# Optimization experiments

Measured on AMD Instinct MI355X. Metric: run time of the kernel, lower is better.

The kernel has to match this reference:

```python
import jax, jax.numpy as jnp
import numpy as np

D_I = 1024
D_O = 1024
B = 4
S = 4096

def setup_inputs() -> dict:
    key = jax.random.key(0)
    kx, kq, kk, kv = jax.random.split(key, 4)
    x = jax.random.normal(kx, (B, S, D_I), dtype=jnp.float32)
    # torch Linear(d_i, d_o) weight is [d_o, d_i]; we store transposed [d_i, d_o]
    sc = 1.0 / np.sqrt(D_I)
    Wq = jax.random.uniform(kq, (D_I, D_O), jnp.float32, -sc, sc)
    Wk = jax.random.uniform(kk, (D_I, D_O), jnp.float32, -sc, sc)
    Wv = jax.random.uniform(kv, (D_I, D_O), jnp.float32, -sc, sc)
    return {"x": x, "Wq": Wq, "Wk": Wk, "Wv": Wv}

def reference(x, Wq, Wk, Wv):
    # x: [B, S, d_i]
    q = jnp.einsum('bsd,de->bse', x, Wq)  # [B,S,d_o]
    k = jnp.einsum('bsd,de->bse', x, Wk)
    v = jnp.einsum('bsd,de->bse', x, Wv)
    scores = jnp.einsum('bqe,bke->bqk', q, k)  # [B,S,S]
    S_len = x.shape[1]
    causal = jnp.tril(jnp.ones((S_len, S_len), dtype=bool))  # keep lower tri
    scores = jnp.where(causal[None], scores, -jnp.inf)
    attn = jax.nn.softmax(scores / jnp.sqrt(jnp.float32(v.shape[-1])), axis=-1)
    # dropout p=0.0 -> identity
    return jnp.einsum('bqk,bke->bqe', attn, v)  # [B,S,d_o]
```

## Files before the change

kernel.cpp:

```cpp
#include <hip/hip_runtime.h>

typedef __bf16 bf16x8 __attribute__((ext_vector_type(8)));
typedef float f32x4 __attribute__((ext_vector_type(4)));

#define B_SZ 4
#define S_SZ 4096
#define D_SZ 1024
#define ELEMS_MAT ((size_t)B_SZ * S_SZ * D_SZ)

#define OFF_Q  ((size_t)0)
#define OFF_K  (ELEMS_MAT)
#define OFF_VT (2 * ELEMS_MAT)
#define ZONE   (3 * ELEMS_MAT)
#define OFF_XB (ZONE)
#define OFF_V  (ZONE + ELEMS_MAT)
#define OFF_WT (ZONE + 2 * ELEMS_MAT)
#define OFF_S  (ZONE)
#define S_BATCH ((size_t)8912896)

#define MFMA16(a, b, c) __builtin_amdgcn_mfma_f32_16x16x32_bf16((a), (b), (c), 0, 0, 0)

static __device__ __forceinline__ unsigned short f2bf(float f) {
  __bf16 h = (__bf16)f;
  return __builtin_bit_cast(unsigned short, h);
}

static __device__ __forceinline__ void async_lds16(const void* g, void* l) {
  __builtin_amdgcn_global_load_lds((__attribute__((address_space(1))) void*)g,
                                   (__attribute__((address_space(3))) void*)l, 16, 0, 0);
}

__global__ void cast_x_kernel(const float* __restrict__ x, unsigned short* __restrict__ xb) {
  size_t i = ((size_t)blockIdx.x * 256 + threadIdx.x) * 8;
  f32x4 a = *(const f32x4*)(x + i);
  f32x4 b = *(const f32x4*)(x + i + 4);
  bf16x8 o;
  o[0] = (__bf16)a[0]; o[1] = (__bf16)a[1]; o[2] = (__bf16)a[2]; o[3] = (__bf16)a[3];
  o[4] = (__bf16)b[0]; o[5] = (__bf16)b[1]; o[6] = (__bf16)b[2]; o[7] = (__bf16)b[3];
  *(bf16x8*)(xb + i) = o;
}

__global__ void cast_wt_kernel(const float* __restrict__ Wq, const float* __restrict__ Wk,
                               const float* __restrict__ Wv, unsigned short* __restrict__ Wt) {
  __shared__ float tl[64][65];
  const float* W = blockIdx.z == 0 ? Wq : (blockIdx.z == 1 ? Wk : Wv);
  unsigned short* out = Wt + (size_t)blockIdx.z * (size_t)D_SZ * (size_t)D_SZ;
  const int k0 = blockIdx.x * 64, n0 = blockIdx.y * 64;
  const int t = threadIdx.x;
  for (int i = t; i < 4096; i += 256) {
    int r = i >> 6, c = i & 63;
    tl[r][c] = W[(size_t)(k0 + r) * D_SZ + n0 + c];
  }
  __syncthreads();
  for (int i = t; i < 4096; i += 256) {
    int r = i >> 6, c = i & 63;
    out[(size_t)(n0 + r) * D_SZ + k0 + c] = f2bf(tl[c][r]);
  }
}

static __device__ __forceinline__ bf16x8 lds_frag(const char* half, int r, int hi) {
  return *(const bf16x8*)(half + r * 64 + ((hi * 16) ^ (((r >> 1) & 3) << 4)));
}

static __device__ __forceinline__ void stage_half256(const char* src, size_t ld, char* lds, int tid) {
#pragma unroll
  for (int it = 0; it < 2; ++it) {
    int i = it * 512 + tid;
    int row = i >> 2;
    int s = (i & 3) ^ ((row >> 1) & 3);
    async_lds16(src + (size_t)row * ld + s * 16, lds + i * 16);
  }
}
static __device__ __forceinline__ void stage_half128(const char* src, size_t ld, char* lds, int tid) {
  int row = tid >> 2;
  int s = (tid & 3) ^ ((row >> 1) & 3);
  async_lds16(src + (size_t)row * ld + s * 16, lds + tid * 16);
}

static __device__ __forceinline__ void mainloop8p(const char* A, size_t lda,
                                                  const char* B, size_t ldb, int NT,
                                                  char sm[2][2][2][16384],
                                                  int tid, f32x4 acc[8][4]) {
  const int lane = tid & 63, w = tid >> 6;
  const int wm = w >> 2, wn = w & 3, lr = lane & 15, hi = lane >> 4;
  stage_half256(A,      lda, sm[0][0][0], tid);
  stage_half256(B,      ldb, sm[0][1][0], tid);
  stage_half256(A + 64, lda, sm[0][0][1], tid);
  stage_half256(B + 64, ldb, sm[0][1][1], tid);
  asm volatile("s_waitcnt vmcnt(4)" ::: "memory");
  __builtin_amdgcn_s_barrier();
  for (int t = 0; t < NT; ++t) {
    const int d = t & 1;
    const char* At1 = A + (size_t)(t + 1) * 128;
    const char* Bt1 = B + (size_t)(t + 1) * 128;
    const bool pre = (t + 1 < NT);
    bf16x8 af[4], bfr[4];
#pragma unroll
    for (int g = 0; g < 4; ++g) bfr[g] = lds_frag(sm[d][1][0], wn * 64 + g * 16 + lr, hi);
#pragma unroll
    for (int f = 0; f < 4; ++f) af[f] = lds_frag(sm[d][0][0], wm * 128 + f * 16 + lr, hi);
    if (pre) stage_half256(At1, lda, sm[d ^ 1][0][0], tid);
    __builtin_amdgcn_s_barrier();
    asm volatile("s_waitcnt lgkmcnt(0)" ::: "memory");
    __builtin_amdgcn_s_setprio(1);
#pragma unroll
    for (int f = 0; f < 4; ++f)
#pragma unroll
      for (int g = 0; g < 4; ++g) acc[f][g] = MFMA16(af[f], bfr[g], acc[f][g]);
    __builtin_amdgcn_s_setprio(0);
    __builtin_amdgcn_s_barrier();
#pragma unroll
    for (int f = 0; f < 4; ++f) af[f] = lds_frag(sm[d][0][0], wm * 128 + 64 + f * 16 + lr, hi);
    if (pre) stage_half256(Bt1, ldb, sm[d ^ 1][1][0], tid);
    __builtin_amdgcn_s_barrier();
    asm volatile("s_waitcnt lgkmcnt(0)" ::: "memory");
    __builtin_amdgcn_s_setprio(1);
#pragma unroll
    for (int f = 0; f < 4; ++f)
#pragma unroll
      for (int g = 0; g < 4; ++g) acc[4 + f][g] = MFMA16(af[f], bfr[g], acc[4 + f][g]);
    __builtin_amdgcn_s_setprio(0);
    if (pre) asm volatile("s_waitcnt vmcnt(4)" ::: "memory");
    else     asm volatile("s_waitcnt vmcnt(0)" ::: "memory");
    __builtin_amdgcn_s_barrier();
#pragma unroll
    for (int g = 0; g < 4; ++g) bfr[g] = lds_frag(sm[d][1][1], wn * 64 + g * 16 + lr, hi);
#pragma unroll
    for (int f = 0; f < 4; ++f) af[f] = lds_frag(sm[d][0][1], wm * 128 + f * 16 + lr, hi);
    if (pre) stage_half256(At1 + 64, lda, sm[d ^ 1][0][1], tid);
    __builtin_amdgcn_s_barrier();
    asm volatile("s_waitcnt lgkmcnt(0)" ::: "memory");
    __builtin_amdgcn_s_setprio(1);
#pragma unroll
    for (int f = 0; f < 4; ++f)
#pragma unroll
      for (int g = 0; g < 4; ++g) acc[f][g] = MFMA16(af[f], bfr[g], acc[f][g]);
    __builtin_amdgcn_s_setprio(0);
    __builtin_amdgcn_s_barrier();
#pragma unroll
    for (int f = 0; f < 4; ++f) af[f] = lds_frag(sm[d][0][1], wm * 128 + 64 + f * 16 + lr, hi);
    if (pre) stage_half256(Bt1 + 64, ldb, sm[d ^ 1][1][1], tid);
    __builtin_amdgcn_s_barrier();
    asm volatile("s_waitcnt lgkmcnt(0)" ::: "memory");
    __builtin_amdgcn_s_setprio(1);
#pragma unroll
    for (int f = 0; f < 4; ++f)
#pragma unroll
      for (int g = 0; g < 4; ++g) acc[4 + f][g] = MFMA16(af[f], bfr[g], acc[4 + f][g]);
    __builtin_amdgcn_s_setprio(0);
    if (pre) asm volatile("s_waitcnt vmcnt(4)" ::: "memory");
    __builtin_amdgcn_s_barrier();
  }
}

#define GEMM_PRE()                                    \
  __shared__ char sm[2][2][2][16384];                 \
  const int tid = threadIdx.x;                        \
  f32x4 acc[8][4];                                    \
  {                                                   \
    const f32x4 z4 = {0.f, 0.f, 0.f, 0.f};            \
    _Pragma("unroll") for (int f = 0; f < 8; ++f)     \
      _Pragma("unroll") for (int g = 0; g < 4; ++g)   \
        acc[f][g] = z4;                               \
  }

#define EPI_IDX()                                     \
  const int lane = tid & 63, w = tid >> 6;            \
  const int wm = w >> 2, wn = w & 3;                  \
  const int lr = lane & 15, hi = lane >> 4;

__global__ __launch_bounds__(512, 2) void gemm_qkv256(const unsigned short* __restrict__ xb,
                                                      const unsigned short* __restrict__ Wt,
                                                      unsigned short* __restrict__ Q,
                                                      unsigned short* __restrict__ K,
                                                      unsigned short* __restrict__ V) {
  GEMM_PRE();
  const int bid = blockIdx.x;
  const int sw = (bid & 7) * 96 + (bid >> 3);
  const int mt = sw % 64, nt = sw / 64;
  const char* A = (const char*)xb + (size_t)mt * 256 * 2048;
  const char* Bp = (const char*)Wt + (size_t)nt * 256 * 2048;
  mainloop8p(A, 2048, Bp, 2048, 16, sm, tid, acc);
  EPI_IDX();
  unsigned short* Out = (nt >> 2) == 0 ? Q : ((nt >> 2) == 1 ? K : V);
  const int nb = (nt & 3) * 256;
#pragma unroll
  for (int f = 0; f < 8; ++f)
#pragma unroll
    for (int g = 0; g < 4; ++g)
#pragma unroll
      for (int j = 0; j < 4; ++j) {
        const int m = mt * 256 + wm * 128 + f * 16 + hi * 4 + j;
        const int n = nb + wn * 64 + g * 16 + lr;
        Out[(size_t)m * D_SZ + n] = f2bf(acc[f][g][j]);
      }
}

__global__ void transpose_v_kernel(const unsigned short* __restrict__ V,
                                   unsigned short* __restrict__ Vt) {
  __shared__ unsigned short tl[64][65];
  const int s0 = blockIdx.x * 64, d0 = blockIdx.y * 64, b = blockIdx.z;
  const int t = threadIdx.x;
  const unsigned short* Vb = V + (size_t)b * S_SZ * D_SZ;
  unsigned short* Vo = Vt + (size_t)b * D_SZ * S_SZ;
  for (int i = t; i < 4096; i += 256) {
    int r = i >> 6, c = i & 63;
    tl[r][c] = Vb[(size_t)(s0 + r) * D_SZ + d0 + c];
  }
  __syncthreads();
  for (int i = t; i < 4096; i += 256) {
    int r = i >> 6, c = i & 63;
    Vo[(size_t)(d0 + r) * S_SZ + s0 + c] = tl[c][r];
  }
}

__global__ __launch_bounds__(512, 2) void s_gemm256(const unsigned short* __restrict__ Q,
                                                    const unsigned short* __restrict__ K,
                                                    unsigned short* __restrict__ Sp) {
  GEMM_PRE();
  const int bid = blockIdx.x;
  const int sw = (bid & 7) * 68 + (bid >> 3);
  const int b = sw / 136;
  const int tile = sw % 136;
  int I = (int)((sqrtf(8.0f * tile + 1.0f) - 1.0f) * 0.5f);
  while ((I + 1) * (I + 2) / 2 <= tile) ++I;
  while (I * (I + 1) / 2 > tile) --I;
  const int J = tile - I * (I + 1) / 2;
  const char* A = (const char*)Q + ((size_t)b * S_SZ + (size_t)I * 256) * 2048;
  const char* Bp = (const char*)K + ((size_t)b * S_SZ + (size_t)J * 256) * 2048;
  mainloop8p(A, 2048, Bp, 2048, 16, sm, tid, acc);
  EPI_IDX();
  const int L = (I + 1) * 256;
  unsigned short* So = Sp + (size_t)b * S_BATCH + (size_t)(I * (I + 1) / 2) * 65536;
#pragma unroll
  for (int f = 0; f < 8; ++f)
#pragma unroll
    for (int g = 0; g < 4; ++g)
#pragma unroll
      for (int j = 0; j < 4; ++j) {
        const int m = wm * 128 + f * 16 + hi * 4 + j;
        const int n = J * 256 + wn * 64 + g * 16 + lr;
        float val = acc[f][g][j] * 0.03125f;
        if (n > I * 256 + m) val = -1e30f;
        So[(size_t)m * L + n] = f2bf(val);
      }
}

__global__ __launch_bounds__(256) void softmax_kernel(unsigned short* __restrict__ Sp) {
  const int w = threadIdx.x >> 6, lane = threadIdx.x & 63;
  const int rowflat = blockIdx.x * 4 + w;
  const int rr = 16383 - rowflat;
  const int b = rr >> 12, q = rr & 4095;
  const int I = q >> 8;
  const int L = (I + 1) << 8;
  unsigned short* base = Sp + (size_t)b * S_BATCH + (size_t)(I * (I + 1) / 2) * 65536 +
                         (size_t)(q & 255) * L;
  const int niter = (L + 511) >> 9;
  const __bf16 NEG = (__bf16)(-1e30f);
  bf16x8 v[8];
#pragma unroll
  for (int jt = 0; jt < 8; ++jt) {
    if (jt < niter) {
      const int off = jt * 512 + lane * 8;
      if (off < L) v[jt] = *(const bf16x8*)(base + off);
      else { bf16x8 fz; fz[0]=NEG;fz[1]=NEG;fz[2]=NEG;fz[3]=NEG;fz[4]=NEG;fz[5]=NEG;fz[6]=NEG;fz[7]=NEG; v[jt] = fz; }
    }
  }
  float m = -1e30f;
#pragma unroll
  for (int jt = 0; jt < 8; ++jt)
    if (jt < niter)
#pragma unroll
      for (int e = 0; e < 8; ++e) m = fmaxf(m, (float)v[jt][e]);
  m = fmaxf(m, __shfl_xor(m, 1));  m = fmaxf(m, __shfl_xor(m, 2));
  m = fmaxf(m, __shfl_xor(m, 4));  m = fmaxf(m, __shfl_xor(m, 8));
  m = fmaxf(m, __shfl_xor(m, 16)); m = fmaxf(m, __shfl_xor(m, 32));
  float l = 0.f;
#pragma unroll
  for (int jt = 0; jt < 8; ++jt)
    if (jt < niter)
#pragma unroll
      for (int e = 0; e < 8; ++e) l += __expf((float)v[jt][e] - m);
  l += __shfl_xor(l, 1);  l += __shfl_xor(l, 2);  l += __shfl_xor(l, 4);
  l += __shfl_xor(l, 8);  l += __shfl_xor(l, 16); l += __shfl_xor(l, 32);
  const float rl = 1.0f / l;
#pragma unroll
  for (int jt = 0; jt < 8; ++jt) {
    if (jt < niter) {
      const int off = jt * 512 + lane * 8;
      if (off < L) {
        bf16x8 p;
#pragma unroll
        for (int e = 0; e < 8; ++e) p[e] = (__bf16)(__expf((float)v[jt][e] - m) * rl);
        *(bf16x8*)(base + off) = p;
      }
    }
  }
}

static __device__ __forceinline__ void mainloop2p128(const char* A, size_t lda,
                                                     const char* B, size_t ldb, int NT,
                                                     char smA[2][2][16384],
                                                     char smB[2][2][8192],
                                                     int tid, f32x4 acc[4][4]) {
  const int lane = tid & 63, w = tid >> 6;
  const int wm = w >> 1, wn = w & 1, lr = lane & 15, hi = lane >> 4;
  stage_half256(A,      lda, smA[0][0], tid);
  stage_half128(B,      ldb, smB[0][0], tid);
  stage_half256(A + 64, lda, smA[0][1], tid);
  stage_half128(B + 64, ldb, smB[0][1], tid);
  asm volatile("s_waitcnt vmcnt(3)" ::: "memory");
  __builtin_amdgcn_s_barrier();
  for (int t = 0; t < NT; ++t) {
    const int d = t & 1;
    const char* At1 = A + (size_t)(t + 1) * 128;
    const char* Bt1 = B + (size_t)(t + 1) * 128;
    const bool pre = (t + 1 < NT);
    bf16x8 af[4], bfr[4];
#pragma unroll
    for (int g = 0; g < 4; ++g) bfr[g] = lds_frag(smB[d][0], wn * 64 + g * 16 + lr, hi);
#pragma unroll
    for (int f = 0; f < 4; ++f) af[f] = lds_frag(smA[d][0], wm * 64 + f * 16 + lr, hi);
    if (pre) { stage_half256(At1, lda, smA[d ^ 1][0], tid); stage_half128(Bt1, ldb, smB[d ^ 1][0], tid); }
    __builtin_amdgcn_s_barrier();
    asm volatile("s_waitcnt lgkmcnt(0)" ::: "memory");
    __builtin_amdgcn_s_setprio(1);
#pragma unroll
    for (int f = 0; f < 4; ++f)
#pragma unroll
      for (int g = 0; g < 4; ++g) acc[f][g] = MFMA16(af[f], bfr[g], acc[f][g]);
    __builtin_amdgcn_s_setprio(0);
    if (pre) asm volatile("s_waitcnt vmcnt(3)" ::: "memory");
    else     asm volatile("s_waitcnt vmcnt(0)" ::: "memory");
    __builtin_amdgcn_s_barrier();
#pragma unroll
    for (int g = 0; g < 4; ++g) bfr[g] = lds_frag(smB[d][1], wn * 64 + g * 16 + lr, hi);
#pragma unroll
    for (int f = 0; f < 4; ++f) af[f] = lds_frag(smA[d][1], wm * 64 + f * 16 + lr, hi);
    if (pre) { stage_half256(At1 + 64, lda, smA[d ^ 1][1], tid); stage_half128(Bt1 + 64, ldb, smB[d ^ 1][1], tid); }
    __builtin_amdgcn_s_barrier();
    asm volatile("s_waitcnt lgkmcnt(0)" ::: "memory");
    __builtin_amdgcn_s_setprio(1);
#pragma unroll
    for (int f = 0; f < 4; ++f)
#pragma unroll
      for (int g = 0; g < 4; ++g) acc[f][g] = MFMA16(af[f], bfr[g], acc[f][g]);
    __builtin_amdgcn_s_setprio(0);
    if (pre) asm volatile("s_waitcnt vmcnt(3)" ::: "memory");
    __builtin_amdgcn_s_barrier();
  }
}

__global__ __launch_bounds__(512, 2) void pv_bal(const unsigned short* __restrict__ Sp,
                                                 const unsigned short* __restrict__ Vt,
                                                 float* __restrict__ out) {
  __shared__ char smA[2][2][16384];
  __shared__ char smB[2][2][8192];
  const int tid = threadIdx.x;
  const int bid = blockIdx.x;
  const int sw = (bid & 7) * 32 + (bid >> 3);
  const int p = sw >> 5, b = (sw >> 3) & 3, nt = sw & 7;
  const int lane = tid & 63, w = tid >> 6;
  const int wm = w >> 1, wn = w & 1;
  const int lr = lane & 15, hi = lane >> 4;
  f32x4 acc[4][4];
#pragma unroll
  for (int half = 0; half < 2; ++half) {
    const int I = half ? (15 - p) : p;
    {
      const f32x4 z4 = {0.f, 0.f, 0.f, 0.f};
#pragma unroll
      for (int f = 0; f < 4; ++f)
#pragma unroll
        for (int g = 0; g < 4; ++g) acc[f][g] = z4;
    }
    const char* A = (const char*)(Sp + (size_t)b * S_BATCH + (size_t)(I * (I + 1) / 2) * 65536);
    const size_t lda = (size_t)(I + 1) * 512;
    const char* Bp = (const char*)Vt + ((size_t)b * D_SZ + (size_t)nt * 128) * (S_SZ * 2);
    mainloop2p128(A, lda, Bp, S_SZ * 2, (I + 1) * 4, smA, smB, tid, acc);
#pragma unroll
    for (int f = 0; f < 4; ++f)
#pragma unroll
      for (int g = 0; g < 4; ++g)
#pragma unroll
        for (int j = 0; j < 4; ++j) {
          const int m = wm * 64 + f * 16 + hi * 4 + j;
          const int n = nt * 128 + wn * 64 + g * 16 + lr;
          out[((size_t)b * S_SZ + (size_t)I * 256 + m) * D_SZ + n] = acc[f][g][j];
        }
    __syncthreads();
  }
}

extern "C" void kernel_launch(void* const* d_in, const int* in_sizes, int n_in,
                              void* d_out, int out_size, void* d_ws, size_t ws_size,
                              hipStream_t stream) {
  (void)in_sizes; (void)n_in; (void)out_size; (void)ws_size;
  const float* x  = (const float*)d_in[0];
  const float* Wq = (const float*)d_in[1];
  const float* Wk = (const float*)d_in[2];
  const float* Wv = (const float*)d_in[3];
  float* out = (float*)d_out;
  unsigned short* ws = (unsigned short*)d_ws;

  cast_x_kernel<<<8192, 256, 0, stream>>>(x, ws + OFF_XB);
  cast_wt_kernel<<<dim3(16, 16, 3), 256, 0, stream>>>(Wq, Wk, Wv, ws + OFF_WT);
  gemm_qkv256<<<768, 512, 0, stream>>>(ws + OFF_XB, ws + OFF_WT,
                                       ws + OFF_Q, ws + OFF_K, ws + OFF_V);
  transpose_v_kernel<<<dim3(64, 16, 4), 256, 0, stream>>>(ws + OFF_V, ws + OFF_VT);
  s_gemm256<<<544, 512, 0, stream>>>(ws + OFF_Q, ws + OFF_K, ws + OFF_S);
  softmax_kernel<<<4096, 256, 0, stream>>>(ws + OFF_S);
  pv_bal<<<256, 512, 0, stream>>>(ws + OFF_S, ws + OFF_VT, out);
}
```

Before: 381.9 us.

## Fuse softmax stats into S GEMM, normalize in PV load, write V transposed

The QKV GEMM epilogue now writes V directly in transposed layout, which removes the separate transpose kernel. The S GEMM computes per-tile row max and sum-exp into partial buffers, and a small merge kernel combines them into a final max and reciprocal sum per row. The PV kernel applies exp and normalization while staging the raw score tiles through registers into LDS, so the standalone softmax pass that read and wrote the full score matrix is gone. In exchange, the async global-to-LDS copies become register-staged loads with extra ALU work inside the PV mainloop, and the stored scores are rounded to bf16 before exponentiation.

```diff
diff --git a/kernel.cpp b/kernel.cpp
--- a/kernel.cpp
+++ b/kernel.cpp
@@ -13,16 +13,20 @@
 #define OFF_VT (2 * ELEMS_MAT)
 #define ZONE   (3 * ELEMS_MAT)
 #define OFF_XB (ZONE)
-#define OFF_V  (ZONE + ELEMS_MAT)
 #define OFF_WT (ZONE + 2 * ELEMS_MAT)
 #define OFF_S  (ZONE)
 #define S_BATCH ((size_t)8912896)
+#define OFF_MP (ZONE + 4 * S_BATCH)
+#define OFF_LP (OFF_MP + 524288)
 
 #define MFMA16(a, b, c) __builtin_amdgcn_mfma_f32_16x16x32_bf16((a), (b), (c), 0, 0, 0)
 
 static __device__ __forceinline__ unsigned short f2bf(float f) {
   __bf16 h = (__bf16)f;
   return __builtin_bit_cast(unsigned short, h);
+}
+static __device__ __forceinline__ float Ef(float x) {
+  return __builtin_exp2f(x * 1.44269504f);
 }
 
 static __device__ __forceinline__ void async_lds16(const void* g, void* l) {
@@ -70,11 +74,6 @@
     int s = (i & 3) ^ ((row >> 1) & 3);
     async_lds16(src + (size_t)row * ld + s * 16, lds + i * 16);
   }
-}
-static __device__ __forceinline__ void stage_half128(const char* src, size_t ld, char* lds, int tid) {
-  int row = tid >> 2;
-  int s = (tid & 3) ^ ((row >> 1) & 3);
-  async_lds16(src + (size_t)row * ld + s * 16, lds + tid * 16);
 }
 
 static __device__ __forceinline__ void mainloop8p(const char* A, size_t lda,
@@ -173,7 +172,7 @@
                                                       const unsigned short* __restrict__ Wt,
                                                       unsigned short* __restrict__ Q,
                                                       unsigned short* __restrict__ K,
-                                                      unsigned short* __restrict__ V) {
+                                                      unsigned short* __restrict__ Vt) {
   GEMM_PRE();
   const int bid = blockIdx.x;
   const int sw = (bid & 7) * 96 + (bid >> 3);
@@ -182,41 +181,40 @@
   const char* Bp = (const char*)Wt + (size_t)nt * 256 * 2048;
   mainloop8p(A, 2048, Bp, 2048, 16, sm, tid, acc);
   EPI_IDX();
-  unsigned short* Out = (nt >> 2) == 0 ? Q : ((nt >> 2) == 1 ? K : V);
-  const int nb = (nt & 3) * 256;
-#pragma unroll
-  for (int f = 0; f < 8; ++f)
-#pragma unroll
-    for (int g = 0; g < 4; ++g)
-#pragma unroll
-      for (int j = 0; j < 4; ++j) {
-        const int m = mt * 256 + wm * 128 + f * 16 + hi * 4 + j;
-        const int n = nb + wn * 64 + g * 16 + lr;
-        Out[(size_t)m * D_SZ + n] = f2bf(acc[f][g][j]);
-      }
-}
-
-__global__ void transpose_v_kernel(const unsigned short* __restrict__ V,
-                                   unsigned short* __restrict__ Vt) {
-  __shared__ unsigned short tl[64][65];
-  const int s0 = blockIdx.x * 64, d0 = blockIdx.y * 64, b = blockIdx.z;
-  const int t = threadIdx.x;
-  const unsigned short* Vb = V + (size_t)b * S_SZ * D_SZ;
-  unsigned short* Vo = Vt + (size_t)b * D_SZ * S_SZ;
-  for (int i = t; i < 4096; i += 256) {
-    int r = i >> 6, c = i & 63;
-    tl[r][c] = Vb[(size_t)(s0 + r) * D_SZ + d0 + c];
-  }
-  __syncthreads();
-  for (int i = t; i < 4096; i += 256) {
-    int r = i >> 6, c = i & 63;
-    Vo[(size_t)(d0 + r) * S_SZ + s0 + c] = tl[c][r];
+  if (nt < 8) {
+    unsigned short* Out = (nt >> 2) == 0 ? Q : K;
+    const int nb = (nt & 3) * 256;
+#pragma unroll
+    for (int f = 0; f < 8; ++f)
+#pragma unroll
+      for (int g = 0; g < 4; ++g)
+#pragma unroll
+        for (int j = 0; j < 4; ++j) {
+          const int m = mt * 256 + wm * 128 + f * 16 + hi * 4 + j;
+          const int n = nb + wn * 64 + g * 16 + lr;
+          Out[(size_t)m * D_SZ + n] = f2bf(acc[f][g][j]);
+        }
+  } else {
+#pragma unroll
+    for (int f = 0; f < 8; ++f)
+#pragma unroll
+      for (int g = 0; g < 4; ++g) {
+        const int m = mt * 256 + wm * 128 + f * 16 + hi * 4;
+        const int n = (nt - 8) * 256 + wn * 64 + g * 16 + lr;
+        const int b = m >> 12, s = m & 4095;
+        ushort4 pk;
+        pk.x = f2bf(acc[f][g][0]); pk.y = f2bf(acc[f][g][1]);
+        pk.z = f2bf(acc[f][g][2]); pk.w = f2bf(acc[f][g][3]);
+        *(ushort4*)(Vt + (size_t)b * (D_SZ * S_SZ) + (size_t)n * S_SZ + s) = pk;
+      }
   }
 }
 
 __global__ __launch_bounds__(512, 2) void s_gemm256(const unsigned short* __restrict__ Q,
                                                     const unsigned short* __restrict__ K,
-                                                    unsigned short* __restrict__ Sp) {
+                                                    unsigned short* __restrict__ Sp,
+                                                    float* __restrict__ mp,
+                                                    float* __restrict__ lp) {
   GEMM_PRE();
   const int bid = blockIdx.x;
   const int sw = (bid & 7) * 68 + (bid >> 3);
@@ -244,115 +242,78 @@
         if (n > I * 256 + m) val = -1e30f;
         So[(size_t)m * L + n] = f2bf(val);
       }
-}
-
-__global__ __launch_bounds__(256) void softmax_kernel(unsigned short* __restrict__ Sp) {
-  const int w = threadIdx.x >> 6, lane = threadIdx.x & 63;
-  const int rowflat = blockIdx.x * 4 + w;
-  const int rr = 16383 - rowflat;
-  const int b = rr >> 12, q = rr & 4095;
-  const int I = q >> 8;
-  const int L = (I + 1) << 8;
-  unsigned short* base = Sp + (size_t)b * S_BATCH + (size_t)(I * (I + 1) / 2) * 65536 +
-                         (size_t)(q & 255) * L;
-  const int niter = (L + 511) >> 9;
-  const __bf16 NEG = (__bf16)(-1e30f);
-  bf16x8 v[8];
-#pragma unroll
-  for (int jt = 0; jt < 8; ++jt) {
-    if (jt < niter) {
-      const int off = jt * 512 + lane * 8;
-      if (off < L) v[jt] = *(const bf16x8*)(base + off);
-      else { bf16x8 fz; fz[0]=NEG;fz[1]=NEG;fz[2]=NEG;fz[3]=NEG;fz[4]=NEG;fz[5]=NEG;fz[6]=NEG;fz[7]=NEG; v[jt] = fz; }
+  float* shm = (float*)sm;
+  float* shl = shm + 1024;
+  __syncthreads();
+#pragma unroll
+  for (int f = 0; f < 8; ++f) {
+#pragma unroll
+    for (int j = 0; j < 4; ++j) {
+      const int m = wm * 128 + f * 16 + hi * 4 + j;
+      float mx = -1e30f;
+#pragma unroll
+      for (int g = 0; g < 4; ++g) {
+        const int n = J * 256 + wn * 64 + g * 16 + lr;
+        float v = acc[f][g][j] * 0.03125f;
+        if (n > I * 256 + m) v = -1e30f;
+        mx = fmaxf(mx, v);
+      }
+      mx = fmaxf(mx, __shfl_xor(mx, 1));
+      mx = fmaxf(mx, __shfl_xor(mx, 2));
+      mx = fmaxf(mx, __shfl_xor(mx, 4));
+      mx = fmaxf(mx, __shfl_xor(mx, 8));
+      float se = 0.f;
+#pragma unroll
+      for (int g = 0; g < 4; ++g) {
+        const int n = J * 256 + wn * 64 + g * 16 + lr;
+        float v = acc[f][g][j] * 0.03125f;
+        if (n > I * 256 + m) v = -1e30f;
+        se += Ef(v - mx);
+      }
+      se += __shfl_xor(se, 1);
+      se += __shfl_xor(se, 2);
+      se += __shfl_xor(se, 4);
+      se += __shfl_xor(se, 8);
+      if (lr == 0) { shm[wn * 256 + m] = mx; shl[wn * 256 + m] = se; }
     }
   }
-  float m = -1e30f;
-#pragma unroll
-  for (int jt = 0; jt < 8; ++jt)
-    if (jt < niter)
-#pragma unroll
-      for (int e = 0; e < 8; ++e) m = fmaxf(m, (float)v[jt][e]);
-  m = fmaxf(m, __shfl_xor(m, 1));  m = fmaxf(m, __shfl_xor(m, 2));
-  m = fmaxf(m, __shfl_xor(m, 4));  m = fmaxf(m, __shfl_xor(m, 8));
-  m = fmaxf(m, __shfl_xor(m, 16)); m = fmaxf(m, __shfl_xor(m, 32));
+  __syncthreads();
+  if (tid < 256) {
+    float m0 = shm[tid], m1 = shm[256 + tid], m2 = shm[512 + tid], m3 = shm[768 + tid];
+    float mm = fmaxf(fmaxf(m0, m1), fmaxf(m2, m3));
+    float ll = shl[tid] * Ef(m0 - mm) + shl[256 + tid] * Ef(m1 - mm) +
+               shl[512 + tid] * Ef(m2 - mm) + shl[768 + tid] * Ef(m3 - mm);
+    const int r = b * 4096 + I * 256 + tid;
+    mp[J * 16384 + r] = mm;
+    lp[J * 16384 + r] = ll;
+  }
+}
+
+__global__ __launch_bounds__(256) void merge_stats(float* __restrict__ mp, float* __restrict__ lp) {
+  const int r = blockIdx.x * 256 + threadIdx.x;
+  const int I = (r & 4095) >> 8;
+  float m = mp[r];
+  for (int J = 1; J <= I; ++J) m = fmaxf(m, mp[J * 16384 + r]);
   float l = 0.f;
-#pragma unroll
-  for (int jt = 0; jt < 8; ++jt)
-    if (jt < niter)
-#pragma unroll
-      for (int e = 0; e < 8; ++e) l += __expf((float)v[jt][e] - m);
-  l += __shfl_xor(l, 1);  l += __shfl_xor(l, 2);  l += __shfl_xor(l, 4);
-  l += __shfl_xor(l, 8);  l += __shfl_xor(l, 16); l += __shfl_xor(l, 32);
-  const float rl = 1.0f / l;
-#pragma unroll
-  for (int jt = 0; jt < 8; ++jt) {
-    if (jt < niter) {
-      const int off = jt * 512 + lane * 8;
-      if (off < L) {
-        bf16x8 p;
-#pragma unroll
-        for (int e = 0; e < 8; ++e) p[e] = (__bf16)(__expf((float)v[jt][e] - m) * rl);
-        *(bf16x8*)(base + off) = p;
-      }
-    }
-  }
-}
-
-static __device__ __forceinline__ void mainloop2p128(const char* A, size_t lda,
-                                                     const char* B, size_t ldb, int NT,
-                                                     char smA[2][2][16384],
-                                                     char smB[2][2][8192],
-                                                     int tid, f32x4 acc[4][4]) {
-  const int lane = tid & 63, w = tid >> 6;
-  const int wm = w >> 1, wn = w & 1, lr = lane & 15, hi = lane >> 4;
-  stage_half256(A,      lda, smA[0][0], tid);
-  stage_half128(B,      ldb, smB[0][0], tid);
-  stage_half256(A + 64, lda, smA[0][1], tid);
-  stage_half128(B + 64, ldb, smB[0][1], tid);
-  asm volatile("s_waitcnt vmcnt(3)" ::: "memory");
-  __builtin_amdgcn_s_barrier();
-  for (int t = 0; t < NT; ++t) {
-    const int d = t & 1;
-    const char* At1 = A + (size_t)(t + 1) * 128;
-    const char* Bt1 = B + (size_t)(t + 1) * 128;
-    const bool pre = (t + 1 < NT);
-    bf16x8 af[4], bfr[4];
-#pragma unroll
-    for (int g = 0; g < 4; ++g) bfr[g] = lds_frag(smB[d][0], wn * 64 + g * 16 + lr, hi);
-#pragma unroll
-    for (int f = 0; f < 4; ++f) af[f] = lds_frag(smA[d][0], wm * 64 + f * 16 + lr, hi);
-    if (pre) { stage_half256(At1, lda, smA[d ^ 1][0], tid); stage_half128(Bt1, ldb, smB[d ^ 1][0], tid); }
-    __builtin_amdgcn_s_barrier();
-    asm volatile("s_waitcnt lgkmcnt(0)" ::: "memory");
-    __builtin_amdgcn_s_setprio(1);
-#pragma unroll
-    for (int f = 0; f < 4; ++f)
-#pragma unroll
-      for (int g = 0; g < 4; ++g) acc[f][g] = MFMA16(af[f], bfr[g], acc[f][g]);
-    __builtin_amdgcn_s_setprio(0);
-    if (pre) asm volatile("s_waitcnt vmcnt(3)" ::: "memory");
-    else     asm volatile("s_waitcnt vmcnt(0)" ::: "memory");
-    __builtin_amdgcn_s_barrier();
-#pragma unroll
-    for (int g = 0; g < 4; ++g) bfr[g] = lds_frag(smB[d][1], wn * 64 + g * 16 + lr, hi);
-#pragma unroll
-    for (int f = 0; f < 4; ++f) af[f] = lds_frag(smA[d][1], wm * 64 + f * 16 + lr, hi);
-    if (pre) { stage_half256(At1 + 64, lda, smA[d ^ 1][1], tid); stage_half128(Bt1 + 64, ldb, smB[d ^ 1][1], tid); }
-    __builtin_amdgcn_s_barrier();
-    asm volatile("s_waitcnt lgkmcnt(0)" ::: "memory");
-    __builtin_amdgcn_s_setprio(1);
-#pragma unroll
-    for (int f = 0; f < 4; ++f)
-#pragma unroll
-      for (int g = 0; g < 4; ++g) acc[f][g] = MFMA16(af[f], bfr[g], acc[f][g]);
-    __builtin_amdgcn_s_setprio(0);
-    if (pre) asm volatile("s_waitcnt vmcnt(3)" ::: "memory");
-    __builtin_amdgcn_s_barrier();
-  }
+  for (int J = 0; J <= I; ++J) l += lp[J * 16384 + r] * Ef(mp[J * 16384 + r] - m);
+  mp[r] = m;
+  lp[r] = 1.0f / l;
+}
+
+static __device__ __forceinline__ bf16x8 xfrm8(bf16x8 v, float m, float rl) {
+  bf16x8 o;
+#pragma unroll
+  for (int e = 0; e < 8; ++e) {
+    float s = (float)v[e];
+    o[e] = (__bf16)(Ef(s - m) * rl);
+  }
+  return o;
 }
 
 __global__ __launch_bounds__(512, 2) void pv_bal(const unsigned short* __restrict__ Sp,
                                                  const unsigned short* __restrict__ Vt,
+                                                 const float* __restrict__ mp,
+                                                 const float* __restrict__ lp,
                                                  float* __restrict__ out) {
   __shared__ char smA[2][2][16384];
   __shared__ char smB[2][2][8192];
@@ -363,6 +324,14 @@
   const int lane = tid & 63, w = tid >> 6;
   const int wm = w >> 1, wn = w & 1;
   const int lr = lane & 15, hi = lane >> 4;
+  const int rA0 = tid >> 2, sA0 = tid & 3;
+  const int rA1 = rA0 + 128, sA1 = sA0;
+  const int rB = tid >> 2, sB = tid & 3;
+  const int wA0 = rA0 * 64 + ((sA0 ^ ((rA0 >> 1) & 3)) << 4);
+  const int wA1 = rA1 * 64 + ((sA1 ^ ((rA1 >> 1) & 3)) << 4);
+  const int wB  = rB  * 64 + ((sB  ^ ((rB  >> 1) & 3)) << 4);
+  const char* Bp = (const char*)Vt + ((size_t)b * D_SZ + (size_t)nt * 128) * (S_SZ * 2);
+
   f32x4 acc[4][4];
 #pragma unroll
   for (int half = 0; half < 2; ++half) {
@@ -374,10 +343,75 @@
 #pragma unroll
         for (int g = 0; g < 4; ++g) acc[f][g] = z4;
     }
-    const char* A = (const char*)(Sp + (size_t)b * S_BATCH + (size_t)(I * (I + 1) / 2) * 65536);
+    const char* Araw = (const char*)(Sp + (size_t)b * S_BATCH + (size_t)(I * (I + 1) / 2) * 65536);
     const size_t lda = (size_t)(I + 1) * 512;
-    const char* Bp = (const char*)Vt + ((size_t)b * D_SZ + (size_t)nt * 128) * (S_SZ * 2);
-    mainloop2p128(A, lda, Bp, S_SZ * 2, (I + 1) * 4, smA, smB, tid, acc);
+    const int NT = (I + 1) * 4;
+    const int rbase = b * 4096 + I * 256;
+    const float m0 = mp[rbase + rA0], rl0 = lp[rbase + rA0];
+    const float m1 = mp[rbase + rA1], rl1 = lp[rbase + rA1];
+
+#define LDA(t, kk, c) (*(const bf16x8*)(Araw + (size_t)(c ? rA1 : rA0) * lda + (size_t)(t) * 128 + (kk) * 64 + (c ? sA1 : sA0) * 16))
+#define LDB(t, kk)    (*(const bf16x8*)(Bp + (size_t)rB * 8192 + (size_t)(t) * 128 + (kk) * 64 + sB * 16))
+
+    {
+      bf16x8 a0 = LDA(0, 0, 0), a1 = LDA(0, 0, 1), b0 = LDB(0, 0);
+      bf16x8 a2 = LDA(0, 1, 0), a3 = LDA(0, 1, 1), b1 = LDB(0, 1);
+      *(bf16x8*)(smA[0][0] + wA0) = xfrm8(a0, m0, rl0);
+      *(bf16x8*)(smA[0][0] + wA1) = xfrm8(a1, m1, rl1);
+      *(bf16x8*)(smB[0][0] + wB) = b0;
+      *(bf16x8*)(smA[0][1] + wA0) = xfrm8(a2, m0, rl0);
+      *(bf16x8*)(smA[0][1] + wA1) = xfrm8(a3, m1, rl1);
+      *(bf16x8*)(smB[0][1] + wB) = b1;
+      asm volatile("s_waitcnt lgkmcnt(0)" ::: "memory");
+      __builtin_amdgcn_s_barrier();
+    }
+    bf16x8 pa0, pa1, pb;
+    bf16x8 qa0, qa1, qb;
+    for (int t = 0; t < NT; ++t) {
+      const int d = t & 1;
+      const bool pre = (t + 1 < NT);
+      bf16x8 af[4], bfr[4];
+#pragma unroll
+      for (int g = 0; g < 4; ++g) bfr[g] = lds_frag(smB[d][0], wn * 64 + g * 16 + lr, hi);
+#pragma unroll
+      for (int f = 0; f < 4; ++f) af[f] = lds_frag(smA[d][0], wm * 64 + f * 16 + lr, hi);
+      if (t > 0) {
+        *(bf16x8*)(smA[d][1] + wA0) = xfrm8(qa0, m0, rl0);
+        *(bf16x8*)(smA[d][1] + wA1) = xfrm8(qa1, m1, rl1);
+        *(bf16x8*)(smB[d][1] + wB) = qb;
+      }
+      if (pre) { pa0 = LDA(t + 1, 0, 0); pa1 = LDA(t + 1, 0, 1); pb = LDB(t + 1, 0); }
+      asm volatile("s_waitcnt lgkmcnt(0)" ::: "memory");
+      __builtin_amdgcn_s_barrier();
+      __builtin_amdgcn_s_setprio(1);
+#pragma unroll
+      for (int f = 0; f < 4; ++f)
+#pragma unroll
+        for (int g = 0; g < 4; ++g) acc[f][g] = MFMA16(af[f], bfr[g], acc[f][g]);
+      __builtin_amdgcn_s_setprio(0);
+      __builtin_amdgcn_s_barrier();
+#pragma unroll
+      for (int g = 0; g < 4; ++g) bfr[g] = lds_frag(smB[d][1], wn * 64 + g * 16 + lr, hi);
+#pragma unroll
+      for (int f = 0; f < 4; ++f) af[f] = lds_frag(smA[d][1], wm * 64 + f * 16 + lr, hi);
+      if (pre) {
+        *(bf16x8*)(smA[d ^ 1][0] + wA0) = xfrm8(pa0, m0, rl0);
+        *(bf16x8*)(smA[d ^ 1][0] + wA1) = xfrm8(pa1, m1, rl1);
+        *(bf16x8*)(smB[d ^ 1][0] + wB) = pb;
+        qa0 = LDA(t + 1, 1, 0); qa1 = LDA(t + 1, 1, 1); qb = LDB(t + 1, 1);
+      }
+      asm volatile("s_waitcnt lgkmcnt(0)" ::: "memory");
+      __builtin_amdgcn_s_barrier();
+      __builtin_amdgcn_s_setprio(1);
+#pragma unroll
+      for (int f = 0; f < 4; ++f)
+#pragma unroll
+        for (int g = 0; g < 4; ++g) acc[f][g] = MFMA16(af[f], bfr[g], acc[f][g]);
+      __builtin_amdgcn_s_setprio(0);
+      __builtin_amdgcn_s_barrier();
+    }
+#undef LDA
+#undef LDB
 #pragma unroll
     for (int f = 0; f < 4; ++f)
 #pragma unroll
@@ -402,13 +436,14 @@
   const float* Wv = (const float*)d_in[3];
   float* out = (float*)d_out;
   unsigned short* ws = (unsigned short*)d_ws;
+  float* mp = (float*)(ws + OFF_MP);
+  float* lp = (float*)(ws + OFF_LP);
 
   cast_x_kernel<<<8192, 256, 0, stream>>>(x, ws + OFF_XB);
   cast_wt_kernel<<<dim3(16, 16, 3), 256, 0, stream>>>(Wq, Wk, Wv, ws + OFF_WT);
   gemm_qkv256<<<768, 512, 0, stream>>>(ws + OFF_XB, ws + OFF_WT,
-                                       ws + OFF_Q, ws + OFF_K, ws + OFF_V);
-  transpose_v_kernel<<<dim3(64, 16, 4), 256, 0, stream>>>(ws + OFF_V, ws + OFF_VT);
-  s_gemm256<<<544, 512, 0, stream>>>(ws + OFF_Q, ws + OFF_K, ws + OFF_S);
-  softmax_kernel<<<4096, 256, 0, stream>>>(ws + OFF_S);
-  pv_bal<<<256, 512, 0, stream>>>(ws + OFF_S, ws + OFF_VT, out);
-}
+                                       ws + OFF_Q, ws + OFF_K, ws + OFF_VT);
+  s_gemm256<<<544, 512, 0, stream>>>(ws + OFF_Q, ws + OFF_K, ws + OFF_S, mp, lp);
+  merge_stats<<<64, 256, 0, stream>>>(mp, lp);
+  pv_bal<<<256, 512, 0, stream>>>(ws + OFF_S, ws + OFF_VT, mp, lp, out);
+}
```

Measured after the change: 457.8 us. +19.9%, slower.
